# Performance work log

Hardware: AMD Instinct MI355X
Metric: run time of the kernel (lower is better)

## Reference

```python
import jax, jax.numpy as jnp
import numpy as np

NODES = 62        # electrodes per graph (hard-coded in model)
BATCH = 2048      # graphs per batch
N = NODES * BATCH # total nodes
IN = 128          # node feature dim (inchannel)
OUT = 62          # ChebConv out channels (hard-coded)
K = 3             # Chebyshev order (config.K)
LIN = 512         # linearsize
HC = 3            # classes (kwargs['HC'])
EPS = 1e-5        # BatchNorm eps
DEG = 4           # out-neighbors per node before symmetrization


def setup_inputs() -> dict:
    key = jax.random.key(0)
    ks = jax.random.split(key, 24)

    # Block-diagonal batched graph: same random 62-node topology per graph, offset per graph.
    rng = np.random.default_rng(0)
    src = np.repeat(np.arange(NODES), DEG)
    dst = (src + 1 + rng.integers(0, NODES - 1, size=src.shape)) % NODES  # no self-loops
    base = np.stack([np.concatenate([src, dst]), np.concatenate([dst, src])])  # [2, e] symmetric
    offs = (np.arange(BATCH) * NODES)[:, None, None]                            # [B,1,1]
    edge_index = (base[None] + offs).transpose(1, 0, 2).reshape(2, -1)          # [2, E]

    in_dims = [IN, IN + OUT, IN + 2 * OUT, IN + 3 * OUT]
    inp = {
        "x": jax.random.normal(ks[0], (N, IN), dtype=jnp.float32),
        "edge_index": jnp.asarray(edge_index, dtype=jnp.int32),
    }
    for i, d in enumerate(in_dims, start=1):
        inp[f"W{i}"] = jax.random.normal(ks[2 * i], (K, d, OUT), dtype=jnp.float32) * (1.0 / np.sqrt(d))
        inp[f"b{i}"] = jnp.zeros((OUT,), dtype=jnp.float32)
    feat = NODES * 4 * OUT  # 15376
    inp["Wh1"] = jax.random.normal(ks[10], (feat, LIN), dtype=jnp.float32) * (1.0 / np.sqrt(feat))
    inp["bh1"] = jnp.zeros((LIN,), dtype=jnp.float32)
    inp["g1"] = jnp.ones((LIN,), dtype=jnp.float32)
    inp["be1"] = jnp.zeros((LIN,), dtype=jnp.float32)
    inp["Wh2"] = jax.random.normal(ks[11], (LIN, LIN // 2), dtype=jnp.float32) * (1.0 / np.sqrt(LIN))
    inp["bh2"] = jnp.zeros((LIN // 2,), dtype=jnp.float32)
    inp["g2"] = jnp.ones((LIN // 2,), dtype=jnp.float32)
    inp["be2"] = jnp.zeros((LIN // 2,), dtype=jnp.float32)
    inp["Wh3"] = jax.random.normal(ks[12], (LIN // 2, HC), dtype=jnp.float32) * (1.0 / np.sqrt(LIN // 2))
    inp["bh3"] = jnp.zeros((HC,), dtype=jnp.float32)
    return inp


def _batchnorm(h, g, b):
    m = h.mean(axis=0)
    v = h.var(axis=0)  # biased, as torch BN training forward
    return (h - m) * jax.lax.rsqrt(v + EPS) * g + b


def reference(x, edge_index, W1, b1, W2, b2, W3, b3, W4, b4,
              Wh1, bh1, g1, be1, Wh2, bh2, g2, be2, Wh3, bh3):
    n = x.shape[0]
    row, col = edge_index[0], edge_index[1]

    # scaled Laplacian L~ = 2L/lambda_max - I = -D^{-1/2} A D^{-1/2} (sym norm, lambda_max=2)
    deg = jax.ops.segment_sum(jnp.ones(row.shape, x.dtype), row, num_segments=n)
    dinv = jnp.where(deg > 0, jnp.where(deg > 0, deg, 1.0) ** -0.5, 0.0)
    w = -(dinv[row] * dinv[col])  # [E]

    def prop(h):  # L~ @ h via edge scatter/gather
        return jax.ops.segment_sum(w[:, None] * h[col], row, num_segments=n)

    def cheb(h, W, b):  # sum_k T_k(L~) h @ W_k + b
        out = h @ W[0]
        Tx0, Tx1 = h, prop(h)
        out = out + Tx1 @ W[1]
        for k in range(2, W.shape[0]):
            Tx2 = 2.0 * prop(Tx1) - Tx0
            out = out + Tx2 @ W[k]
            Tx0, Tx1 = Tx1, Tx2
        return out + b

    relu = jax.nn.relu
    x1 = relu(cheb(x, W1, b1))
    x2 = relu(cheb(jnp.concatenate([x, x1], axis=1), W2, b2))
    x3 = relu(cheb(jnp.concatenate([x, x1, x2], axis=1), W3, b3))
    x4 = relu(cheb(jnp.concatenate([x, x1, x2, x3], axis=1), W4, b4))

    feats = jnp.concatenate([x1, x2, x3, x4], axis=1)        # [N, 4*OUT]
    feats = feats.reshape(BATCH, -1)                          # [B, 62*4*OUT] (attention==identity)

    h = relu(_batchnorm(feats @ Wh1 + bh1, g1, be1))          # dropout: identity (eval)
    h = relu(_batchnorm(h @ Wh2 + bh2, g2, be2))
    logits = h @ Wh3 + bh3
    return jax.nn.softmax(logits, axis=1)
```

## Files before the change

### kernel.cpp

```cpp
#include <hip/hip_runtime.h>


#define NODES   62
#define BATCH   2048
#define NTOT    (NODES * BATCH)
#define IN_DIM  128
#define OUT_DIM 62
#define ACOLS   248
#define FEAT    15376
#define LIN1    512
#define LIN2    256
#define NCLS    3
#define BN_EPS  1e-5f

typedef __attribute__((ext_vector_type(8)))  short  short8;
typedef __attribute__((ext_vector_type(4)))  float  f32x4;
typedef __attribute__((ext_vector_type(16))) float  f32x16;
typedef __attribute__((ext_vector_type(4)))  unsigned short us4;

__device__ inline unsigned short f2bf(float x) {
    unsigned u = __builtin_bit_cast(unsigned, x);
    return (unsigned short)((u + 0x7fffu + ((u >> 16) & 1u)) >> 16);
}
__device__ inline float bf2f(unsigned short h) {
    return __builtin_bit_cast(float, (unsigned)h << 16);
}
__device__ inline void tsplit(float x, unsigned short& hi, unsigned short& lo) {
    unsigned u = __builtin_bit_cast(unsigned, x);
    hi = (unsigned short)(u >> 16);
    float r = x - __builtin_bit_cast(float, u & 0xffff0000u);
    lo = (unsigned short)(__builtin_bit_cast(unsigned, r) >> 16);
}
__device__ inline int fo(int r, int k) {
    return (((r + 2 * k) & 15) + 16 * k) * 8;
}

#define PREP_GRID 11153
__global__ __launch_bounds__(256) void prep_kernel(
    const int* __restrict__ ei, int E, int epg, unsigned short* __restrict__ Tf,
    const float* __restrict__ W1, const float* __restrict__ W2,
    const float* __restrict__ W3, const float* __restrict__ W4,
    unsigned short* __restrict__ WTall,
    const float* __restrict__ Wh1, unsigned short* __restrict__ Wh1T,
    float* __restrict__ H1, const float* __restrict__ bh1,
    float* __restrict__ H2, const float* __restrict__ bh2)
{
    __shared__ __align__(16) char ps[48640];
    const int bid = blockIdx.x;
    const int t   = threadIdx.x;

    if (bid == 0) {
        float* Ls   = (float*)ps;
        float* Ts   = (float*)(ps + 15376);
        int*   deg  = (int*)(ps + 48144);
        float* dinv = (float*)(ps + 48392);
        for (int i = t; i < NODES * NODES; i += 256) Ls[i] = 0.f;
        if (t < NODES) deg[t] = 0;
        __syncthreads();
        const int* row = ei;
        const int* col = ei + E;
        for (int j = t; j < epg; j += 256) atomicAdd(&deg[row[j]], 1);
        __syncthreads();
        if (t < NODES) dinv[t] = (deg[t] > 0) ? rsqrtf((float)deg[t]) : 0.f;
        __syncthreads();
        for (int j = t; j < epg; j += 256) {
            int r = row[j], c = col[j];
            atomicAdd(&Ls[r * NODES + c], -dinv[r] * dinv[c]);
        }
        __syncthreads();
        for (int idx = t; idx < 4096; idx += 256) {
            int r = idx >> 6, c = idx & 63;
            float t1 = 0.f, t2 = 0.f;
            if (r < NODES && c < NODES) {
                t1 = Ls[r * NODES + c];
                float s = 0.f;
                for (int j = 0; j < NODES; ++j) s += Ls[r * NODES + j] * Ls[j * NODES + c];
                t2 = 2.f * s - (r == c ? 1.f : 0.f);
            }
            Ts[idx]        = t1;
            Ts[4096 + idx] = t2;
        }
        __syncthreads();
        for (int idx = t; idx < 16384; idx += 256) {
            int j    = idx & 7;
            int lane = (idx >> 3) & 63;
            int pl   = (idx >> 9) & 1;
            int ks   = (idx >> 10) & 3;
            int w    = (idx >> 12) & 3;
            int m = (w & 1) * 32 + (lane & 31);
            int k = ks * 16 + (lane >> 5) * 8 + j;
            float v = Ts[(w >> 1) * 4096 + m * 64 + k];
            unsigned short hi, lo;
            tsplit(v, hi, lo);
            Tf[idx] = pl ? lo : hi;
        }
    } else if (bid < 1921) {
        const int li    = bid - 1;
        const int layer = li / 480;
        const int bx    = li - layer * 480;
        const float* W = (layer == 0) ? W1 : (layer == 1) ? W2 : (layer == 2) ? W3 : W4;
        const int d    = (layer == 0) ? 128 : (layer == 1) ? 190 : (layer == 2) ? 252 : 314;
        const int dpad = (layer == 0) ? 128 : (layer == 1) ? 192 : (layer == 2) ? 256 : 320;
        const int cum  = (layer == 0) ? 0 : (layer == 1) ? 4 : (layer == 2) ? 10 : 18;
        unsigned short* WTf = WTall + (size_t)cum * 12288;
        const int total = (dpad >> 5) * 12288;
        int idx = bx * 256 + t;
        if (idx >= total) return;
        int j    = idx & 7;
        int lane = (idx >> 3) & 63;
        int f    = idx >> 9;
        int nt   = f & 1;
        int pl   = (f >> 1) & 1;
        int ks   = (f >> 2) & 1;
        int seg  = (f >> 3) % 3;
        int ch   = (f >> 3) / 3;
        int n  = nt * 32 + (lane & 31);
        int kk = ch * 32 + ks * 16 + (lane >> 5) * 8 + j;
        float v = (n < NODES && kk < d) ? W[((size_t)seg * d + kk) * OUT_DIM + n] : 0.f;
        unsigned short hi, lo;
        tsplit(v, hi, lo);
        WTf[idx] = pl ? lo : hi;
    } else if (bid < 9617) {
        const int ti = bid - 1921;
        const int k0 = (ti % 481) * 32;
        const int n0 = (ti / 481) * 32;
        float (*T)[33] = (float(*)[33])ps;
        {
            int kl = t >> 3, n4 = (t & 7) * 4;
            if (k0 + kl < FEAT) {
                float4 v = *(const float4*)&Wh1[(size_t)(k0 + kl) * LIN1 + n0 + n4];
                T[kl][n4] = v.x; T[kl][n4 + 1] = v.y; T[kl][n4 + 2] = v.z; T[kl][n4 + 3] = v.w;
            }
        }
        __syncthreads();
        {
            int nl = t >> 3, k4 = (t & 7) * 4;
            if (k0 + k4 + 3 < FEAT) {
                ushort4 o;
                o.x = f2bf(T[k4 + 0][nl]);
                o.y = f2bf(T[k4 + 1][nl]);
                o.z = f2bf(T[k4 + 2][nl]);
                o.w = f2bf(T[k4 + 3][nl]);
                *(ushort4*)&Wh1T[(size_t)(n0 + nl) * FEAT + k0 + k4] = o;
            }
        }
    } else {
        const int i = (bid - 9617) * 256 + t;
        const int n1 = BATCH * LIN1 / 4;
        if (i < n1) {
            ((float4*)H1)[i] = ((const float4*)bh1)[i & (LIN1 / 4 - 1)];
        } else {
            int j = i - n1;
            ((float4*)H2)[j] = ((const float4*)bh2)[j & (LIN2 / 4 - 1)];
        }
    }
}

__global__ __launch_bounds__(256, 4) void cheb_mfma(
    const float* __restrict__ x, float* __restrict__ X248,
    const unsigned short* __restrict__ WTf, const unsigned short* __restrict__ Tf,
    const float* __restrict__ bias, int d, int dpad)
{
    __shared__ __align__(16) unsigned short smem[17408];
    __shared__ float bias_s[64];

    unsigned short* hA = smem;
    unsigned short* Bs = smem + 5120;

    const int tid  = threadIdx.x;
    const int g    = blockIdx.x;
    const int lane = tid & 63;
    const int wv   = tid >> 6;
    const int mtw  = wv >> 1, ntw = wv & 1;

    if (tid < 64) bias_s[tid] = (tid < OUT_DIM) ? bias[tid] : 0.f;

    const int srow = tid >> 2;
    const int scg  = (tid & 3) * 8;

    const int nchunk = dpad >> 5;

    f32x16 acc[3];
    #pragma unroll
    for (int s = 0; s < 3; ++s)
        #pragma unroll
        for (int i = 0; i < 16; ++i) acc[s][i] = 0.f;

    float  vh[8];
    short8 breg[6];

#define LOADCH(cn)                                                             \
    do {                                                                       \
        const int gf_ = (cn) * 32 + scg;                                       \
        if (srow < NODES) {                                                    \
            if ((cn) * 32 < IN_DIM) {                                          \
                const float4* p_ = (const float4*)&x[(size_t)(g * NODES + srow) * IN_DIM + gf_]; \
                float4 a_ = p_[0], b_ = p_[1];                                 \
                vh[0] = a_.x; vh[1] = a_.y; vh[2] = a_.z; vh[3] = a_.w;        \
                vh[4] = b_.x; vh[5] = b_.y; vh[6] = b_.z; vh[7] = b_.w;        \
            } else if (gf_ + 8 <= d) {                                         \
                const float4* p_ = (const float4*)&X248[(size_t)(g * NODES + srow) * ACOLS + (gf_ - IN_DIM)]; \
                float4 a_ = p_[0], b_ = p_[1];                                 \
                vh[0] = a_.x; vh[1] = a_.y; vh[2] = a_.z; vh[3] = a_.w;        \
                vh[4] = b_.x; vh[5] = b_.y; vh[6] = b_.z; vh[7] = b_.w;        \
            } else {                                                           \
                _Pragma("unroll")                                              \
                for (int p = 0; p < 8; ++p)                                    \
                    vh[p] = (gf_ + p < d)                                      \
                        ? X248[(size_t)(g * NODES + srow) * ACOLS + (gf_ - IN_DIM) + p] : 0.f; \
            }                                                                  \
        } else {                                                               \
            _Pragma("unroll")                                                  \
            for (int p = 0; p < 8; ++p) vh[p] = 0.f;                           \
        }                                                                      \
        const short8* wsrc_ = (const short8*)(WTf + (size_t)(cn) * 12288);     \
        _Pragma("unroll")                                                      \
        for (int i = 0; i < 6; ++i) breg[i] = wsrc_[i * 256 + tid];            \
    } while (0)

    LOADCH(0);

    for (int ch = 0; ch < nchunk; ++ch) {
        {
            short8 hi8, lo8;
            #pragma unroll
            for (int p = 0; p < 8; ++p) {
                unsigned short h_, l_;
                tsplit(vh[p], h_, l_);
                hi8[p] = (short)h_; lo8[p] = (short)l_;
            }
            *(short8*)&hA[srow * 40 + scg]        = hi8;
            *(short8*)&hA[2560 + srow * 40 + scg] = lo8;
            #pragma unroll
            for (int i = 0; i < 6; ++i) ((short8*)Bs)[i * 256 + tid] = breg[i];
        }
        __syncthreads();
        if (ch + 1 < nchunk) LOADCH(ch + 1);
        {
            const int arow = mtw * 32 + (lane & 31);
            const int akf  = (lane >> 5) * 8;
            #pragma unroll
            for (int ks = 0; ks < 2; ++ks) {
                short8 ahi = *(const short8*)&hA[arow * 40 + ks * 16 + akf];
                short8 alo = *(const short8*)&hA[2560 + arow * 40 + ks * 16 + akf];
                #pragma unroll
                for (int seg = 0; seg < 3; ++seg) {
                    const unsigned short* bp =
                        Bs + ((((seg * 2 + ks) * 2 + 0) * 2 + ntw) << 9) + lane * 8;
                    short8 bhi = *(const short8*)bp;
                    short8 blo = *(const short8*)(bp + 1024);
                    acc[seg] = __builtin_amdgcn_mfma_f32_32x32x16_bf16(ahi, bhi, acc[seg], 0, 0, 0);
                    acc[seg] = __builtin_amdgcn_mfma_f32_32x32x16_bf16(ahi, blo, acc[seg], 0, 0, 0);
                    acc[seg] = __builtin_amdgcn_mfma_f32_32x32x16_bf16(alo, bhi, acc[seg], 0, 0, 0);
                }
            }
        }
        __syncthreads();
    }
#undef LOADCH

    short8 Tr[2][4][2];
    #pragma unroll
    for (int mat = 0; mat < 2; ++mat) {
        const int w = mat * 2 + mtw;
        #pragma unroll
        for (int ks = 0; ks < 4; ++ks)
            #pragma unroll
            for (int pl = 0; pl < 2; ++pl)
                Tr[mat][ks][pl] =
                    *(const short8*)(Tf + (((size_t)(w * 4 + ks) * 2 + pl) << 9) + lane * 8);
    }
    {
        const int jb = (lane >> 5) * 4;
        const int lq = lane & 31;
        #pragma unroll
        for (int q = 0; q < 4; ++q) {
            const int ks2 = mtw * 2 + (q >> 1);
            const int lp  = lq + 32 * (q & 1);
            us4 s1h, s1l, s2h, s2l;
            #pragma unroll
            for (int r = 0; r < 4; ++r) {
                unsigned short hi_, lo_;
                tsplit(acc[1][q * 4 + r], hi_, lo_);
                s1h[r] = hi_; s1l[r] = lo_;
                tsplit(acc[2][q * 4 + r], hi_, lo_);
                s2h[r] = hi_; s2l[r] = lo_;
            }
            const int base = lp * 8 + jb;
            *(us4*)&smem[((((0 + ks2) * 2 + 0) * 2 + ntw) << 9) + base] = s1h;
            *(us4*)&smem[((((0 + ks2) * 2 + 1) * 2 + ntw) << 9) + base] = s1l;
            *(us4*)&smem[((((4 + ks2) * 2 + 0) * 2 + ntw) << 9) + base] = s2h;
            *(us4*)&smem[((((4 + ks2) * 2 + 1) * 2 + ntw) << 9) + base] = s2l;
        }
    }
    __syncthreads();
    f32x16 out = acc[0];
    #pragma unroll
    for (int mat = 0; mat < 2; ++mat)
        #pragma unroll
        for (int ks = 0; ks < 4; ++ks) {
            const unsigned short* sp =
                smem + ((((mat * 4 + ks) * 2 + 0) * 2 + ntw) << 9) + lane * 8;
            short8 shi = *(const short8*)sp;
            short8 slo = *(const short8*)(sp + 1024);
            out = __builtin_amdgcn_mfma_f32_32x32x16_bf16(Tr[mat][ks][0], shi, out, 0, 0, 0);
            out = __builtin_amdgcn_mfma_f32_32x32x16_bf16(Tr[mat][ks][0], slo, out, 0, 0, 0);
            out = __builtin_amdgcn_mfma_f32_32x32x16_bf16(Tr[mat][ks][1], shi, out, 0, 0, 0);
        }
    {
        const int c = ntw * 32 + (lane & 31);
        if (c < OUT_DIM) {
            const int mbase = mtw * 32 + 4 * (lane >> 5);
            #pragma unroll
            for (int reg = 0; reg < 16; ++reg) {
                int m = mbase + (reg & 3) + 8 * (reg >> 2);
                if (m < NODES) {
                    float v = fmaxf(out[reg] + bias_s[c], 0.f);
                    X248[(size_t)(g * NODES + m) * ACOLS + (d - IN_DIM) + c] = v;
                }
            }
        }
    }
}

#define SPLIT1 8
__global__ __launch_bounds__(256) void gemm_head1_mfma(
    const float* __restrict__ F32, const unsigned short* __restrict__ WT1,
    float* __restrict__ H1)
{
    __shared__ __align__(16) unsigned short A16[4 * 512];
    __shared__ __align__(16) unsigned short B16[8 * 512];
    const int tid  = threadIdx.x;
    const int lane = tid & 63;
    const int wv   = tid >> 6;
    const int bm = blockIdx.x, bnb = blockIdx.y, s = blockIdx.z;
    const int c0 = (481 * s) / SPLIT1, c1 = (481 * (s + 1)) / SPLIT1;
    const int mr = tid >> 2, kg = (tid & 3) * 8;
    const int mrB = tid >> 1, kgB = (tid & 1) * 16;
    const int aoff  = (mr >> 4) * 512 + fo(mr & 15, tid & 3);
    const int boff0 = (mrB >> 4) * 512 + fo(mrB & 15, (tid & 1) * 2);
    const int boff1 = (mrB >> 4) * 512 + fo(mrB & 15, (tid & 1) * 2 + 1);
    const int roff  = fo(lane & 15, lane >> 4);

    f32x4 acc[8];
    #pragma unroll
    for (int i = 0; i < 8; ++i) acc[i] = (f32x4){0.f, 0.f, 0.f, 0.f};

    float4 u0, u1;
    short8 bv0, bv1;
#define LOAD1(cn)                                                              \
    do {                                                                       \
        const int k_ = (cn) * 32 + kg;                                         \
        u0 = (float4){0.f, 0.f, 0.f, 0.f};                                     \
        u1 = (float4){0.f, 0.f, 0.f, 0.f};                                     \
        bv0 = (short8){0, 0, 0, 0, 0, 0, 0, 0};                                \
        bv1 = (short8){0, 0, 0, 0, 0, 0, 0, 0};                                \
        if (k_ + 8 <= FEAT) {                                                  \
            const float4* p_ = (const float4*)&F32[(size_t)(bm * 64 + mr) * FEAT + k_]; \
            u0 = p_[0]; u1 = p_[1];                                            \
        }                                                                      \
        const int kB_ = (cn) * 32 + kgB;                                       \
        if (kB_ + 8 <= FEAT)                                                   \
            bv0 = *(const short8*)&WT1[(size_t)(bnb * 128 + mrB) * FEAT + kB_]; \
        if (kB_ + 16 <= FEAT)                                                  \
            bv1 = *(const short8*)&WT1[(size_t)(bnb * 128 + mrB) * FEAT + kB_ + 8]; \
    } while (0)

    LOAD1(c0);
    for (int ch = c0; ch < c1; ++ch) {
        {
            short8 av;
            av[0] = (short)f2bf(u0.x); av[1] = (short)f2bf(u0.y);
            av[2] = (short)f2bf(u0.z); av[3] = (short)f2bf(u0.w);
            av[4] = (short)f2bf(u1.x); av[5] = (short)f2bf(u1.y);
            av[6] = (short)f2bf(u1.z); av[7] = (short)f2bf(u1.w);
            *(short8*)&A16[aoff]  = av;
            *(short8*)&B16[boff0] = bv0;
            *(short8*)&B16[boff1] = bv1;
        }
        __syncthreads();
        if (ch + 1 < c1) LOAD1(ch + 1);
        short8 af = *(short8*)&A16[wv * 512 + roff];
        #pragma unroll
        for (int nt = 0; nt < 8; ++nt) {
            short8 bf = *(short8*)&B16[nt * 512 + roff];
            acc[nt] = __builtin_amdgcn_mfma_f32_16x16x32_bf16(af, bf, acc[nt], 0, 0, 0);
        }
        __syncthreads();
    }
#undef LOAD1
    const int m0 = bm * 64 + wv * 16 + (lane >> 4) * 4;
    #pragma unroll
    for (int nt = 0; nt < 8; ++nt) {
        int c = bnb * 128 + nt * 16 + (lane & 15);
        #pragma unroll
        for (int rg = 0; rg < 4; ++rg)
            atomicAdd(&H1[(size_t)(m0 + rg) * LIN1 + c], acc[nt][rg]);
    }
}

#define ACC16(av, bv) do {                              \
    acc[0][0] = fmaf((av).x, (bv).x, acc[0][0]);        \
    acc[0][1] = fmaf((av).x, (bv).y, acc[0][1]);        \
    acc[0][2] = fmaf((av).x, (bv).z, acc[0][2]);        \
    acc[0][3] = fmaf((av).x, (bv).w, acc[0][3]);        \
    acc[1][0] = fmaf((av).y, (bv).x, acc[1][0]);        \
    acc[1][1] = fmaf((av).y, (bv).y, acc[1][1]);        \
    acc[1][2] = fmaf((av).y, (bv).z, acc[1][2]);        \
    acc[1][3] = fmaf((av).y, (bv).w, acc[1][3]);        \
    acc[2][0] = fmaf((av).z, (bv).x, acc[2][0]);        \
    acc[2][1] = fmaf((av).z, (bv).y, acc[2][1]);        \
    acc[2][2] = fmaf((av).z, (bv).z, acc[2][2]);        \
    acc[2][3] = fmaf((av).z, (bv).w, acc[2][3]);        \
    acc[3][0] = fmaf((av).w, (bv).x, acc[3][0]);        \
    acc[3][1] = fmaf((av).w, (bv).y, acc[3][1]);        \
    acc[3][2] = fmaf((av).w, (bv).z, acc[3][2]);        \
    acc[3][3] = fmaf((av).w, (bv).w, acc[3][3]);        \
} while (0)

#define SPLIT2 4
__global__ __launch_bounds__(256) void gemm2_kernel(
    const float* __restrict__ A, const float* __restrict__ B,
    float* __restrict__ C)
{
    __shared__ __align__(16) float As[16 * 72];
    __shared__ __align__(16) float Bs[16 * 64];
    const int bm = blockIdx.x, bnb = blockIdx.y, s = blockIdx.z;
    const int tid = threadIdx.x;
    const int ty4 = (tid >> 4) * 4;
    const int tx4 = (tid & 15) * 4;
    const int kbeg = s * (LIN1 / SPLIT2);
    const int kend = kbeg + LIN1 / SPLIT2;
    float acc[4][4] = {};
    for (int k0 = kbeg; k0 < kend; k0 += 16) {
        for (int i = tid; i < 1024; i += 256) {
            int m = i >> 4, kt = i & 15;
            As[kt * 72 + m] = A[(size_t)(bm * 64 + m) * LIN1 + k0 + kt];
        }
        for (int i = tid; i < 1024; i += 256) {
            int kt = i >> 6, c = i & 63;
            Bs[kt * 64 + c] = B[(size_t)(k0 + kt) * LIN2 + bnb * 64 + c];
        }
        __syncthreads();
        #pragma unroll
        for (int kt = 0; kt < 16; ++kt) {
            const float4 av = *(const float4*)&As[kt * 72 + ty4];
            const float4 bv = *(const float4*)&Bs[kt * 64 + tx4];
            ACC16(av, bv);
        }
        __syncthreads();
    }
    const int b = bm * 64 + ty4, c = bnb * 64 + tx4;
    #pragma unroll
    for (int i = 0; i < 4; ++i)
        #pragma unroll
        for (int j = 0; j < 4; ++j)
            atomicAdd(&C[(size_t)(b + i) * LIN2 + c + j], acc[i][j]);
}

__global__ __launch_bounds__(256) void bn_relu_kernel(
    float* __restrict__ H, int C,
    const float* __restrict__ gamma, const float* __restrict__ beta)
{
    const int c  = blockIdx.x * 16 + (threadIdx.x & 15);
    const int rt = threadIdx.x >> 4;
    const int ct = threadIdx.x & 15;
    float s = 0.f, s2 = 0.f;
    for (int r = rt; r < BATCH; r += 16) {
        float v = H[(size_t)r * C + c];
        s += v; s2 += v * v;
    }
    __shared__ float Ss[16][16], S2s[16][16], sc_s[16], sh_s[16];
    Ss[rt][ct] = s; S2s[rt][ct] = s2;
    __syncthreads();
    if (rt == 0) {
        float ts = 0.f, ts2 = 0.f;
        #pragma unroll
        for (int i = 0; i < 16; ++i) { ts += Ss[i][ct]; ts2 += S2s[i][ct]; }
        float m   = ts * (1.f / BATCH);
        float var = ts2 * (1.f / BATCH) - m * m;
        float sc  = gamma[c] * rsqrtf(var + BN_EPS);
        sc_s[ct] = sc;
        sh_s[ct] = beta[c] - m * sc;
    }
    __syncthreads();
    const float sc = sc_s[ct], sh = sh_s[ct];
    for (int r = rt; r < BATCH; r += 16) {
        float v = H[(size_t)r * C + c];
        H[(size_t)r * C + c] = fmaxf(fmaf(v, sc, sh), 0.f);
    }
}

__global__ __launch_bounds__(256) void final_kernel(
    const float* __restrict__ H2, const float* __restrict__ Wh3,
    const float* __restrict__ bh3, float* __restrict__ out)
{
    __shared__ float Ws[LIN2 * NCLS];
    __shared__ float bs[NCLS];
    const int tid = threadIdx.x;
    for (int i = tid; i < LIN2 * NCLS; i += 256) Ws[i] = Wh3[i];
    if (tid < NCLS) bs[tid] = bh3[tid];
    __syncthreads();
    const int r = blockIdx.x * 256 + tid;
    float a0 = bs[0], a1 = bs[1], a2 = bs[2];
    const float4* row = (const float4*)&H2[(size_t)r * LIN2];
    for (int k4 = 0; k4 < LIN2 / 4; ++k4) {
        float4 h = row[k4];
        int k = k4 * 4;
        a0 = fmaf(h.x, Ws[(k + 0) * 3 + 0], a0);
        a1 = fmaf(h.x, Ws[(k + 0) * 3 + 1], a1);
        a2 = fmaf(h.x, Ws[(k + 0) * 3 + 2], a2);
        a0 = fmaf(h.y, Ws[(k + 1) * 3 + 0], a0);
        a1 = fmaf(h.y, Ws[(k + 1) * 3 + 1], a1);
        a2 = fmaf(h.y, Ws[(k + 1) * 3 + 2], a2);
        a0 = fmaf(h.z, Ws[(k + 2) * 3 + 0], a0);
        a1 = fmaf(h.z, Ws[(k + 2) * 3 + 1], a1);
        a2 = fmaf(h.z, Ws[(k + 2) * 3 + 2], a2);
        a0 = fmaf(h.w, Ws[(k + 3) * 3 + 0], a0);
        a1 = fmaf(h.w, Ws[(k + 3) * 3 + 1], a1);
        a2 = fmaf(h.w, Ws[(k + 3) * 3 + 2], a2);
    }
    float mx = fmaxf(a0, fmaxf(a1, a2));
    float e0 = expf(a0 - mx), e1 = expf(a1 - mx), e2 = expf(a2 - mx);
    float inv = 1.f / (e0 + e1 + e2);
    out[r * 3 + 0] = e0 * inv;
    out[r * 3 + 1] = e1 * inv;
    out[r * 3 + 2] = e2 * inv;
}

extern "C" void kernel_launch(void* const* d_in, const int* in_sizes, int n_in,
                              void* d_out, int out_size, void* d_ws, size_t ws_size,
                              hipStream_t stream)
{
    const float* x   = (const float*)d_in[0];
    const int*   ei  = (const int*)  d_in[1];
    const float* W1  = (const float*)d_in[2];
    const float* b1  = (const float*)d_in[3];
    const float* W2  = (const float*)d_in[4];
    const float* b2  = (const float*)d_in[5];
    const float* W3  = (const float*)d_in[6];
    const float* b3  = (const float*)d_in[7];
    const float* W4  = (const float*)d_in[8];
    const float* b4  = (const float*)d_in[9];
    const float* Wh1 = (const float*)d_in[10];
    const float* bh1 = (const float*)d_in[11];
    const float* g1  = (const float*)d_in[12];
    const float* be1 = (const float*)d_in[13];
    const float* Wh2 = (const float*)d_in[14];
    const float* bh2 = (const float*)d_in[15];
    const float* g2  = (const float*)d_in[16];
    const float* be2 = (const float*)d_in[17];
    const float* Wh3 = (const float*)d_in[18];
    const float* bh3 = (const float*)d_in[19];
    float* out = (float*)d_out;

    char* ws = (char*)d_ws;
    unsigned short* Tf    = (unsigned short*)(ws + 32768);
    unsigned short* WTall = (unsigned short*)(ws + 65536);
    unsigned short* Wh1T  = (unsigned short*)(ws + 753664);
    float* X248 = (float*)(ws + 16498688);
    float* H1   = (float*)(ws + 142458880);
    float* H2   = (float*)(ws + 146653184);

    const int E   = in_sizes[1] / 2;
    const int epg = E / BATCH;

    prep_kernel<<<PREP_GRID, 256, 0, stream>>>(
        ei, E, epg, Tf, W1, W2, W3, W4, WTall, Wh1, Wh1T, H1, bh1, H2, bh2);

    cheb_mfma<<<BATCH, 256, 0, stream>>>(x, X248, WTall + (size_t)0 * 12288,  Tf, b1, 128, 128);
    cheb_mfma<<<BATCH, 256, 0, stream>>>(x, X248, WTall + (size_t)4 * 12288,  Tf, b2, 190, 192);
    cheb_mfma<<<BATCH, 256, 0, stream>>>(x, X248, WTall + (size_t)10 * 12288, Tf, b3, 252, 256);
    cheb_mfma<<<BATCH, 256, 0, stream>>>(x, X248, WTall + (size_t)18 * 12288, Tf, b4, 314, 320);

    gemm_head1_mfma<<<dim3(32, 4, SPLIT1), 256, 0, stream>>>(X248, Wh1T, H1);
    bn_relu_kernel<<<LIN1 / 16, 256, 0, stream>>>(H1, LIN1, g1, be1);

    gemm2_kernel<<<dim3(32, 4, SPLIT2), 256, 0, stream>>>(H1, Wh2, H2);
    bn_relu_kernel<<<LIN2 / 16, 256, 0, stream>>>(H2, LIN2, g2, be2);

    final_kernel<<<BATCH / 256, 256, 0, stream>>>(H2, Wh3, bh3, out);
}
```

Measured before the change: 639.6 us.

## Fuse four ChebConv layer launches into one per-graph kernel

Replaces the four separate cheb_mfma launches with a single cheb_fused4 kernel that loops over the four layers inside each graph's block, loading all four biases up front. This removes three kernel launches and their inter-kernel drains, and lets each block's earlier-layer outputs in X248 likely still sit in cache when the next layer reads them. The layer loop is unrolled, which may raise code size and register pressure. Correctness relies on each block only reading the X248 rows it wrote itself, with the end-of-layer barrier making them visible.

```diff
diff --git a/kernel.cpp b/kernel.cpp
--- a/kernel.cpp
+++ b/kernel.cpp
@@ -156,13 +156,14 @@
     }
 }
 
-__global__ __launch_bounds__(256, 4) void cheb_mfma(
+__global__ __launch_bounds__(256, 4) void cheb_fused4(
     const float* __restrict__ x, float* __restrict__ X248,
-    const unsigned short* __restrict__ WTf, const unsigned short* __restrict__ Tf,
-    const float* __restrict__ bias, int d, int dpad)
+    const unsigned short* __restrict__ WTall, const unsigned short* __restrict__ Tf,
+    const float* __restrict__ b1, const float* __restrict__ b2,
+    const float* __restrict__ b3, const float* __restrict__ b4)
 {
     __shared__ __align__(16) unsigned short smem[17408];
-    __shared__ float bias_s[64];
+    __shared__ float bias_s[256];
 
     unsigned short* hA = smem;
     unsigned short* Bs = smem + 5120;
@@ -173,21 +174,31 @@
     const int wv   = tid >> 6;
     const int mtw  = wv >> 1, ntw = wv & 1;
 
-    if (tid < 64) bias_s[tid] = (tid < OUT_DIM) ? bias[tid] : 0.f;
+    {
+        const int ll = tid >> 6, c = tid & 63;
+        const float* bp = (ll == 0) ? b1 : (ll == 1) ? b2 : (ll == 2) ? b3 : b4;
+        bias_s[tid] = (c < OUT_DIM) ? bp[c] : 0.f;
+    }
+    __syncthreads();
 
     const int srow = tid >> 2;
     const int scg  = (tid & 3) * 8;
 
-    const int nchunk = dpad >> 5;
-
-    f32x16 acc[3];
     #pragma unroll
-    for (int s = 0; s < 3; ++s)
-        #pragma unroll
-        for (int i = 0; i < 16; ++i) acc[s][i] = 0.f;
-
-    float  vh[8];
-    short8 breg[6];
+    for (int l = 0; l < 4; ++l) {
+        const int d      = (l == 0) ? 128 : (l == 1) ? 190 : (l == 2) ? 252 : 314;
+        const int nchunk = (l == 0) ? 4   : (l == 1) ? 6   : (l == 2) ? 8   : 10;
+        const unsigned short* WTf =
+            WTall + (size_t)((l == 0) ? 0 : (l == 1) ? 4 : (l == 2) ? 10 : 18) * 12288;
+
+        f32x16 acc[3];
+        #pragma unroll
+        for (int s = 0; s < 3; ++s)
+            #pragma unroll
+            for (int i = 0; i < 16; ++i) acc[s][i] = 0.f;
+
+        float  vh[8];
+        short8 breg[6];
 
 #define LOADCH(cn)                                                             \
     do {                                                                       \
@@ -218,108 +229,111 @@
         for (int i = 0; i < 6; ++i) breg[i] = wsrc_[i * 256 + tid];            \
     } while (0)
 
-    LOADCH(0);
-
-    for (int ch = 0; ch < nchunk; ++ch) {
+        LOADCH(0);
+
+        for (int ch = 0; ch < nchunk; ++ch) {
+            {
+                short8 hi8, lo8;
+                #pragma unroll
+                for (int p = 0; p < 8; ++p) {
+                    unsigned short h_, l_;
+                    tsplit(vh[p], h_, l_);
+                    hi8[p] = (short)h_; lo8[p] = (short)l_;
+                }
+                *(short8*)&hA[srow * 40 + scg]        = hi8;
+                *(short8*)&hA[2560 + srow * 40 + scg] = lo8;
+                #pragma unroll
+                for (int i = 0; i < 6; ++i) ((short8*)Bs)[i * 256 + tid] = breg[i];
+            }
+            __syncthreads();
+            if (ch + 1 < nchunk) LOADCH(ch + 1);
+            {
+                const int arow = mtw * 32 + (lane & 31);
+                const int akf  = (lane >> 5) * 8;
+                #pragma unroll
+                for (int ks = 0; ks < 2; ++ks) {
+                    short8 ahi = *(const short8*)&hA[arow * 40 + ks * 16 + akf];
+                    short8 alo = *(const short8*)&hA[2560 + arow * 40 + ks * 16 + akf];
+                    #pragma unroll
+                    for (int seg = 0; seg < 3; ++seg) {
+                        const unsigned short* bp =
+                            Bs + ((((seg * 2 + ks) * 2 + 0) * 2 + ntw) << 9) + lane * 8;
+                        short8 bhi = *(const short8*)bp;
+                        short8 blo = *(const short8*)(bp + 1024);
+                        acc[seg] = __builtin_amdgcn_mfma_f32_32x32x16_bf16(ahi, bhi, acc[seg], 0, 0, 0);
+                        acc[seg] = __builtin_amdgcn_mfma_f32_32x32x16_bf16(ahi, blo, acc[seg], 0, 0, 0);
+                        acc[seg] = __builtin_amdgcn_mfma_f32_32x32x16_bf16(alo, bhi, acc[seg], 0, 0, 0);
+                    }
+                }
+            }
+            __syncthreads();
+        }
+#undef LOADCH
+
+        short8 Tr[2][4][2];
+        #pragma unroll
+        for (int mat = 0; mat < 2; ++mat) {
+            const int w = mat * 2 + mtw;
+            #pragma unroll
+            for (int ks = 0; ks < 4; ++ks)
+                #pragma unroll
+                for (int pl = 0; pl < 2; ++pl)
+                    Tr[mat][ks][pl] =
+                        *(const short8*)(Tf + (((size_t)(w * 4 + ks) * 2 + pl) << 9) + lane * 8);
+        }
         {
-            short8 hi8, lo8;
+            const int jb = (lane >> 5) * 4;
+            const int lq = lane & 31;
             #pragma unroll
-            for (int p = 0; p < 8; ++p) {
-                unsigned short h_, l_;
-                tsplit(vh[p], h_, l_);
-                hi8[p] = (short)h_; lo8[p] = (short)l_;
-            }
-            *(short8*)&hA[srow * 40 + scg]        = hi8;
-            *(short8*)&hA[2560 + srow * 40 + scg] = lo8;
+            for (int q = 0; q < 4; ++q) {
+                const int ks2 = mtw * 2 + (q >> 1);
+                const int lp  = lq + 32 * (q & 1);
+                us4 s1h, s1l, s2h, s2l;
+                #pragma unroll
+                for (int r = 0; r < 4; ++r) {
+                    unsigned short hi_, lo_;
+                    tsplit(acc[1][q * 4 + r], hi_, lo_);
+                    s1h[r] = hi_; s1l[r] = lo_;
+                    tsplit(acc[2][q * 4 + r], hi_, lo_);
+                    s2h[r] = hi_; s2l[r] = lo_;
+                }
+                const int base = lp * 8 + jb;
+                *(us4*)&smem[((((0 + ks2) * 2 + 0) * 2 + ntw) << 9) + base] = s1h;
+                *(us4*)&smem[((((0 + ks2) * 2 + 1) * 2 + ntw) << 9) + base] = s1l;
+                *(us4*)&smem[((((4 + ks2) * 2 + 0) * 2 + ntw) << 9) + base] = s2h;
+                *(us4*)&smem[((((4 + ks2) * 2 + 1) * 2 + ntw) << 9) + base] = s2l;
+            }
+        }
+        __syncthreads();
+        f32x16 outv = acc[0];
+        #pragma unroll
+        for (int mat = 0; mat < 2; ++mat)
             #pragma unroll
-            for (int i = 0; i < 6; ++i) ((short8*)Bs)[i * 256 + tid] = breg[i];
-        }
-        __syncthreads();
-        if (ch + 1 < nchunk) LOADCH(ch + 1);
+            for (int ks = 0; ks < 4; ++ks) {
+                const unsigned short* sp =
+                    smem + ((((mat * 4 + ks) * 2 + 0) * 2 + ntw) << 9) + lane * 8;
+                short8 shi = *(const short8*)sp;
+                short8 slo = *(const short8*)(sp + 1024);
+                outv = __builtin_amdgcn_mfma_f32_32x32x16_bf16(Tr[mat][ks][0], shi, outv, 0, 0, 0);
+                outv = __builtin_amdgcn_mfma_f32_32x32x16_bf16(Tr[mat][ks][0], slo, outv, 0, 0, 0);
+                outv = __builtin_amdgcn_mfma_f32_32x32x16_bf16(Tr[mat][ks][1], shi, outv, 0, 0, 0);
+            }
         {
-            const int arow = mtw * 32 + (lane & 31);
-            const int akf  = (lane >> 5) * 8;
-            #pragma unroll
-            for (int ks = 0; ks < 2; ++ks) {
-                short8 ahi = *(const short8*)&hA[arow * 40 + ks * 16 + akf];
-                short8 alo = *(const short8*)&hA[2560 + arow * 40 + ks * 16 + akf];
+            const int c = ntw * 32 + (lane & 31);
+            if (c < OUT_DIM) {
+                const float bv = bias_s[l * 64 + c];
+                const int mbase = mtw * 32 + 4 * (lane >> 5);
                 #pragma unroll
-                for (int seg = 0; seg < 3; ++seg) {
-                    const unsigned short* bp =
-                        Bs + ((((seg * 2 + ks) * 2 + 0) * 2 + ntw) << 9) + lane * 8;
-                    short8 bhi = *(const short8*)bp;
-                    short8 blo = *(const short8*)(bp + 1024);
-                    acc[seg] = __builtin_amdgcn_mfma_f32_32x32x16_bf16(ahi, bhi, acc[seg], 0, 0, 0);
-                    acc[seg] = __builtin_amdgcn_mfma_f32_32x32x16_bf16(ahi, blo, acc[seg], 0, 0, 0);
-                    acc[seg] = __builtin_amdgcn_mfma_f32_32x32x16_bf16(alo, bhi, acc[seg], 0, 0, 0);
+                for (int reg = 0; reg < 16; ++reg) {
+                    int m = mbase + (reg & 3) + 8 * (reg >> 2);
+                    if (m < NODES) {
+                        float v = fmaxf(outv[reg] + bv, 0.f);
+                        X248[(size_t)(g * NODES + m) * ACOLS + 62 * l + c] = v;
+                    }
                 }
             }
         }
         __syncthreads();
-    }
-#undef LOADCH
-
-    short8 Tr[2][4][2];
-    #pragma unroll
-    for (int mat = 0; mat < 2; ++mat) {
-        const int w = mat * 2 + mtw;
-        #pragma unroll
-        for (int ks = 0; ks < 4; ++ks)
-            #pragma unroll
-            for (int pl = 0; pl < 2; ++pl)
-                Tr[mat][ks][pl] =
-                    *(const short8*)(Tf + (((size_t)(w * 4 + ks) * 2 + pl) << 9) + lane * 8);
-    }
-    {
-        const int jb = (lane >> 5) * 4;
-        const int lq = lane & 31;
-        #pragma unroll
-        for (int q = 0; q < 4; ++q) {
-            const int ks2 = mtw * 2 + (q >> 1);
-            const int lp  = lq + 32 * (q & 1);
-            us4 s1h, s1l, s2h, s2l;
-            #pragma unroll
-            for (int r = 0; r < 4; ++r) {
-                unsigned short hi_, lo_;
-                tsplit(acc[1][q * 4 + r], hi_, lo_);
-                s1h[r] = hi_; s1l[r] = lo_;
-                tsplit(acc[2][q * 4 + r], hi_, lo_);
-                s2h[r] = hi_; s2l[r] = lo_;
-            }
-            const int base = lp * 8 + jb;
-            *(us4*)&smem[((((0 + ks2) * 2 + 0) * 2 + ntw) << 9) + base] = s1h;
-            *(us4*)&smem[((((0 + ks2) * 2 + 1) * 2 + ntw) << 9) + base] = s1l;
-            *(us4*)&smem[((((4 + ks2) * 2 + 0) * 2 + ntw) << 9) + base] = s2h;
-            *(us4*)&smem[((((4 + ks2) * 2 + 1) * 2 + ntw) << 9) + base] = s2l;
-        }
-    }
-    __syncthreads();
-    f32x16 out = acc[0];
-    #pragma unroll
-    for (int mat = 0; mat < 2; ++mat)
-        #pragma unroll
-        for (int ks = 0; ks < 4; ++ks) {
-            const unsigned short* sp =
-                smem + ((((mat * 4 + ks) * 2 + 0) * 2 + ntw) << 9) + lane * 8;
-            short8 shi = *(const short8*)sp;
-            short8 slo = *(const short8*)(sp + 1024);
-            out = __builtin_amdgcn_mfma_f32_32x32x16_bf16(Tr[mat][ks][0], shi, out, 0, 0, 0);
-            out = __builtin_amdgcn_mfma_f32_32x32x16_bf16(Tr[mat][ks][0], slo, out, 0, 0, 0);
-            out = __builtin_amdgcn_mfma_f32_32x32x16_bf16(Tr[mat][ks][1], shi, out, 0, 0, 0);
-        }
-    {
-        const int c = ntw * 32 + (lane & 31);
-        if (c < OUT_DIM) {
-            const int mbase = mtw * 32 + 4 * (lane >> 5);
-            #pragma unroll
-            for (int reg = 0; reg < 16; ++reg) {
-                int m = mbase + (reg & 3) + 8 * (reg >> 2);
-                if (m < NODES) {
-                    float v = fmaxf(out[reg] + bias_s[c], 0.f);
-                    X248[(size_t)(g * NODES + m) * ACOLS + (d - IN_DIM) + c] = v;
-                }
-            }
-        }
     }
 }
 
@@ -568,10 +582,7 @@
     prep_kernel<<<PREP_GRID, 256, 0, stream>>>(
         ei, E, epg, Tf, W1, W2, W3, W4, WTall, Wh1, Wh1T, H1, bh1, H2, bh2);
 
-    cheb_mfma<<<BATCH, 256, 0, stream>>>(x, X248, WTall + (size_t)0 * 12288,  Tf, b1, 128, 128);
-    cheb_mfma<<<BATCH, 256, 0, stream>>>(x, X248, WTall + (size_t)4 * 12288,  Tf, b2, 190, 192);
-    cheb_mfma<<<BATCH, 256, 0, stream>>>(x, X248, WTall + (size_t)10 * 12288, Tf, b3, 252, 256);
-    cheb_mfma<<<BATCH, 256, 0, stream>>>(x, X248, WTall + (size_t)18 * 12288, Tf, b4, 314, 320);
+    cheb_fused4<<<BATCH, 256, 0, stream>>>(x, X248, WTall, Tf, b1, b2, b3, b4);
 
     gemm_head1_mfma<<<dim3(32, 4, SPLIT1), 256, 0, stream>>>(X248, Wh1T, H1);
     bn_relu_kernel<<<LIN1 / 16, 256, 0, stream>>>(H1, LIN1, g1, be1);
```

Result: no change. 647.0 us (+1.2%).

## Split BatchNorm into parallel stats pass and fuse normalize+ReLU into consumers

Applied to the files above, without the earlier changes.

Replaces each bn_relu kernel, which ran few blocks and read and rewrote H in place, with a bn_stats kernel that spreads rows over 16x more blocks and accumulates per-column sums atomically. The normalize+ReLU is applied on the fly when gemm2 loads A and when final_kernel reads H2, so the in-place write pass disappears. final_kernel is also reorganized to use 8 threads per row with shuffle reductions, giving more parallelism. The stats buffers are zeroed by two extra blocks in prep_kernel, which adds atomics and a workspace dependency.

```diff
diff --git a/kernel.cpp b/kernel.cpp
--- a/kernel.cpp
+++ b/kernel.cpp
@@ -35,7 +35,7 @@
     return (((r + 2 * k) & 15) + 16 * k) * 8;
 }
 
-#define PREP_GRID 11153
+#define PREP_GRID 11155
 __global__ __launch_bounds__(256) void prep_kernel(
     const int* __restrict__ ei, int E, int epg, unsigned short* __restrict__ Tf,
     const float* __restrict__ W1, const float* __restrict__ W2,
@@ -43,7 +43,8 @@
     unsigned short* __restrict__ WTall,
     const float* __restrict__ Wh1, unsigned short* __restrict__ Wh1T,
     float* __restrict__ H1, const float* __restrict__ bh1,
-    float* __restrict__ H2, const float* __restrict__ bh2)
+    float* __restrict__ H2, const float* __restrict__ bh2,
+    float* __restrict__ stats)
 {
     __shared__ __align__(16) char ps[48640];
     const int bid = blockIdx.x;
@@ -147,11 +148,16 @@
     } else {
         const int i = (bid - 9617) * 256 + t;
         const int n1 = BATCH * LIN1 / 4;
+        const int n2 = BATCH * LIN2 / 4;
         if (i < n1) {
             ((float4*)H1)[i] = ((const float4*)bh1)[i & (LIN1 / 4 - 1)];
-        } else {
+        } else if (i - n1 < n2) {
             int j = i - n1;
             ((float4*)H2)[j] = ((const float4*)bh2)[j & (LIN2 / 4 - 1)];
+        } else {
+            int j = i - n1 - n2;
+            if (j < 512)
+                ((float4*)stats)[j] = (float4){0.f, 0.f, 0.f, 0.f};
         }
     }
 }
@@ -399,6 +405,31 @@
     }
 }
 
+__global__ __launch_bounds__(256) void bn_stats(
+    const float* __restrict__ H, int C,
+    float* __restrict__ Sg, float* __restrict__ S2g)
+{
+    const int ct = threadIdx.x & 15;
+    const int rt = threadIdx.x >> 4;
+    const int c  = blockIdx.x * 16 + ct;
+    const int r0 = blockIdx.y * 16 + rt;
+    float s = 0.f, s2 = 0.f;
+    for (int r = r0; r < BATCH; r += 256) {
+        float v = H[(size_t)r * C + c];
+        s += v; s2 += v * v;
+    }
+    __shared__ float Ss[16][17], S2s[16][17];
+    Ss[rt][ct] = s; S2s[rt][ct] = s2;
+    __syncthreads();
+    if (rt == 0) {
+        float ts = 0.f, ts2 = 0.f;
+        #pragma unroll
+        for (int i = 0; i < 16; ++i) { ts += Ss[i][ct]; ts2 += S2s[i][ct]; }
+        atomicAdd(&Sg[c], ts);
+        atomicAdd(&S2g[c], ts2);
+    }
+}
+
 #define ACC16(av, bv) do {                              \
     acc[0][0] = fmaf((av).x, (bv).x, acc[0][0]);        \
     acc[0][1] = fmaf((av).x, (bv).y, acc[0][1]);        \
@@ -421,21 +452,35 @@
 #define SPLIT2 4
 __global__ __launch_bounds__(256) void gemm2_kernel(
     const float* __restrict__ A, const float* __restrict__ B,
-    float* __restrict__ C)
+    float* __restrict__ C,
+    const float* __restrict__ Sg1, const float* __restrict__ S2g1,
+    const float* __restrict__ g1, const float* __restrict__ be1)
 {
     __shared__ __align__(16) float As[16 * 72];
     __shared__ __align__(16) float Bs[16 * 64];
+    __shared__ float scs[128], shs[128];
     const int bm = blockIdx.x, bnb = blockIdx.y, s = blockIdx.z;
     const int tid = threadIdx.x;
     const int ty4 = (tid >> 4) * 4;
     const int tx4 = (tid & 15) * 4;
     const int kbeg = s * (LIN1 / SPLIT2);
     const int kend = kbeg + LIN1 / SPLIT2;
+    if (tid < 128) {
+        const int k = kbeg + tid;
+        float mn  = Sg1[k] * (1.f / BATCH);
+        float var = S2g1[k] * (1.f / BATCH) - mn * mn;
+        float sc  = g1[k] * rsqrtf(var + BN_EPS);
+        scs[tid] = sc;
+        shs[tid] = be1[k] - mn * sc;
+    }
+    __syncthreads();
     float acc[4][4] = {};
     for (int k0 = kbeg; k0 < kend; k0 += 16) {
         for (int i = tid; i < 1024; i += 256) {
             int m = i >> 4, kt = i & 15;
-            As[kt * 72 + m] = A[(size_t)(bm * 64 + m) * LIN1 + k0 + kt];
+            float raw = A[(size_t)(bm * 64 + m) * LIN1 + k0 + kt];
+            int kl = k0 + kt - kbeg;
+            As[kt * 72 + m] = fmaxf(fmaf(raw, scs[kl], shs[kl]), 0.f);
         }
         for (int i = tid; i < 1024; i += 256) {
             int kt = i >> 6, c = i & 63;
@@ -458,74 +503,68 @@
             atomicAdd(&C[(size_t)(b + i) * LIN2 + c + j], acc[i][j]);
 }
 
-__global__ __launch_bounds__(256) void bn_relu_kernel(
-    float* __restrict__ H, int C,
-    const float* __restrict__ gamma, const float* __restrict__ beta)
-{
-    const int c  = blockIdx.x * 16 + (threadIdx.x & 15);
-    const int rt = threadIdx.x >> 4;
-    const int ct = threadIdx.x & 15;
-    float s = 0.f, s2 = 0.f;
-    for (int r = rt; r < BATCH; r += 16) {
-        float v = H[(size_t)r * C + c];
-        s += v; s2 += v * v;
-    }
-    __shared__ float Ss[16][16], S2s[16][16], sc_s[16], sh_s[16];
-    Ss[rt][ct] = s; S2s[rt][ct] = s2;
-    __syncthreads();
-    if (rt == 0) {
-        float ts = 0.f, ts2 = 0.f;
-        #pragma unroll
-        for (int i = 0; i < 16; ++i) { ts += Ss[i][ct]; ts2 += S2s[i][ct]; }
-        float m   = ts * (1.f / BATCH);
-        float var = ts2 * (1.f / BATCH) - m * m;
-        float sc  = gamma[c] * rsqrtf(var + BN_EPS);
-        sc_s[ct] = sc;
-        sh_s[ct] = beta[c] - m * sc;
-    }
-    __syncthreads();
-    const float sc = sc_s[ct], sh = sh_s[ct];
-    for (int r = rt; r < BATCH; r += 16) {
-        float v = H[(size_t)r * C + c];
-        H[(size_t)r * C + c] = fmaxf(fmaf(v, sc, sh), 0.f);
-    }
-}
-
 __global__ __launch_bounds__(256) void final_kernel(
     const float* __restrict__ H2, const float* __restrict__ Wh3,
-    const float* __restrict__ bh3, float* __restrict__ out)
+    const float* __restrict__ bh3, float* __restrict__ out,
+    const float* __restrict__ Sg2, const float* __restrict__ S2g2,
+    const float* __restrict__ g2, const float* __restrict__ be2)
 {
     __shared__ float Ws[LIN2 * NCLS];
     __shared__ float bs[NCLS];
+    __shared__ float sc2[LIN2], sh2[LIN2];
     const int tid = threadIdx.x;
     for (int i = tid; i < LIN2 * NCLS; i += 256) Ws[i] = Wh3[i];
     if (tid < NCLS) bs[tid] = bh3[tid];
+    {
+        float mn  = Sg2[tid] * (1.f / BATCH);
+        float var = S2g2[tid] * (1.f / BATCH) - mn * mn;
+        float sc  = g2[tid] * rsqrtf(var + BN_EPS);
+        sc2[tid] = sc;
+        sh2[tid] = be2[tid] - mn * sc;
+    }
     __syncthreads();
-    const int r = blockIdx.x * 256 + tid;
-    float a0 = bs[0], a1 = bs[1], a2 = bs[2];
+    const int r     = blockIdx.x * 32 + (tid >> 3);
+    const int lane8 = tid & 7;
+    float a0 = (lane8 == 0) ? bs[0] : 0.f;
+    float a1 = (lane8 == 0) ? bs[1] : 0.f;
+    float a2 = (lane8 == 0) ? bs[2] : 0.f;
     const float4* row = (const float4*)&H2[(size_t)r * LIN2];
-    for (int k4 = 0; k4 < LIN2 / 4; ++k4) {
+    #pragma unroll
+    for (int i = 0; i < 8; ++i) {
+        const int k4 = lane8 + i * 8;
         float4 h = row[k4];
-        int k = k4 * 4;
-        a0 = fmaf(h.x, Ws[(k + 0) * 3 + 0], a0);
-        a1 = fmaf(h.x, Ws[(k + 0) * 3 + 1], a1);
-        a2 = fmaf(h.x, Ws[(k + 0) * 3 + 2], a2);
-        a0 = fmaf(h.y, Ws[(k + 1) * 3 + 0], a0);
-        a1 = fmaf(h.y, Ws[(k + 1) * 3 + 1], a1);
-        a2 = fmaf(h.y, Ws[(k + 1) * 3 + 2], a2);
-        a0 = fmaf(h.z, Ws[(k + 2) * 3 + 0], a0);
-        a1 = fmaf(h.z, Ws[(k + 2) * 3 + 1], a1);
-        a2 = fmaf(h.z, Ws[(k + 2) * 3 + 2], a2);
-        a0 = fmaf(h.w, Ws[(k + 3) * 3 + 0], a0);
-        a1 = fmaf(h.w, Ws[(k + 3) * 3 + 1], a1);
-        a2 = fmaf(h.w, Ws[(k + 3) * 3 + 2], a2);
-    }
-    float mx = fmaxf(a0, fmaxf(a1, a2));
-    float e0 = expf(a0 - mx), e1 = expf(a1 - mx), e2 = expf(a2 - mx);
-    float inv = 1.f / (e0 + e1 + e2);
-    out[r * 3 + 0] = e0 * inv;
-    out[r * 3 + 1] = e1 * inv;
-    out[r * 3 + 2] = e2 * inv;
+        const int k = k4 * 4;
+        float h0 = fmaxf(fmaf(h.x, sc2[k + 0], sh2[k + 0]), 0.f);
+        float h1 = fmaxf(fmaf(h.y, sc2[k + 1], sh2[k + 1]), 0.f);
+        float h2v = fmaxf(fmaf(h.z, sc2[k + 2], sh2[k + 2]), 0.f);
+        float h3 = fmaxf(fmaf(h.w, sc2[k + 3], sh2[k + 3]), 0.f);
+        a0 = fmaf(h0, Ws[(k + 0) * 3 + 0], a0);
+        a1 = fmaf(h0, Ws[(k + 0) * 3 + 1], a1);
+        a2 = fmaf(h0, Ws[(k + 0) * 3 + 2], a2);
+        a0 = fmaf(h1, Ws[(k + 1) * 3 + 0], a0);
+        a1 = fmaf(h1, Ws[(k + 1) * 3 + 1], a1);
+        a2 = fmaf(h1, Ws[(k + 1) * 3 + 2], a2);
+        a0 = fmaf(h2v, Ws[(k + 2) * 3 + 0], a0);
+        a1 = fmaf(h2v, Ws[(k + 2) * 3 + 1], a1);
+        a2 = fmaf(h2v, Ws[(k + 2) * 3 + 2], a2);
+        a0 = fmaf(h3, Ws[(k + 3) * 3 + 0], a0);
+        a1 = fmaf(h3, Ws[(k + 3) * 3 + 1], a1);
+        a2 = fmaf(h3, Ws[(k + 3) * 3 + 2], a2);
+    }
+    #pragma unroll
+    for (int m = 1; m < 8; m <<= 1) {
+        a0 += __shfl_xor(a0, m);
+        a1 += __shfl_xor(a1, m);
+        a2 += __shfl_xor(a2, m);
+    }
+    if (lane8 == 0) {
+        float mx = fmaxf(a0, fmaxf(a1, a2));
+        float e0 = expf(a0 - mx), e1 = expf(a1 - mx), e2 = expf(a2 - mx);
+        float inv = 1.f / (e0 + e1 + e2);
+        out[r * 3 + 0] = e0 * inv;
+        out[r * 3 + 1] = e1 * inv;
+        out[r * 3 + 2] = e2 * inv;
+    }
 }
 
 extern "C" void kernel_launch(void* const* d_in, const int* in_sizes, int n_in,
@@ -555,6 +594,10 @@
     float* out = (float*)d_out;
 
     char* ws = (char*)d_ws;
+    float* Sg1  = (float*)(ws + 0);
+    float* S2g1 = (float*)(ws + 2048);
+    float* Sg2  = (float*)(ws + 4096);
+    float* S2g2 = (float*)(ws + 5120);
     unsigned short* Tf    = (unsigned short*)(ws + 32768);
     unsigned short* WTall = (unsigned short*)(ws + 65536);
     unsigned short* Wh1T  = (unsigned short*)(ws + 753664);
@@ -566,7 +609,8 @@
     const int epg = E / BATCH;
 
     prep_kernel<<<PREP_GRID, 256, 0, stream>>>(
-        ei, E, epg, Tf, W1, W2, W3, W4, WTall, Wh1, Wh1T, H1, bh1, H2, bh2);
+        ei, E, epg, Tf, W1, W2, W3, W4, WTall, Wh1, Wh1T, H1, bh1, H2, bh2,
+        (float*)ws);
 
     cheb_mfma<<<BATCH, 256, 0, stream>>>(x, X248, WTall + (size_t)0 * 12288,  Tf, b1, 128, 128);
     cheb_mfma<<<BATCH, 256, 0, stream>>>(x, X248, WTall + (size_t)4 * 12288,  Tf, b2, 190, 192);
@@ -574,10 +618,9 @@
     cheb_mfma<<<BATCH, 256, 0, stream>>>(x, X248, WTall + (size_t)18 * 12288, Tf, b4, 314, 320);
 
     gemm_head1_mfma<<<dim3(32, 4, SPLIT1), 256, 0, stream>>>(X248, Wh1T, H1);
-    bn_relu_kernel<<<LIN1 / 16, 256, 0, stream>>>(H1, LIN1, g1, be1);
-
-    gemm2_kernel<<<dim3(32, 4, SPLIT2), 256, 0, stream>>>(H1, Wh2, H2);
-    bn_relu_kernel<<<LIN2 / 16, 256, 0, stream>>>(H2, LIN2, g2, be2);
-
-    final_kernel<<<BATCH / 256, 256, 0, stream>>>(H2, Wh3, bh3, out);
-}
+
+    bn_stats<<<dim3(LIN1 / 16, 16), 256, 0, stream>>>(H1, LIN1, Sg1, S2g1);
+    gemm2_kernel<<<dim3(32, 4, SPLIT2), 256, 0, stream>>>(H1, Wh2, H2, Sg1, S2g1, g1, be1);
+    bn_stats<<<dim3(LIN2 / 16, 16), 256, 0, stream>>>(H2, LIN2, Sg2, S2g2);
+    final_kernel<<<BATCH / 32, 256, 0, stream>>>(H2, Wh3, bh3, out, Sg2, S2g2, g2, be2);
+}
```

After: 518.8 us. -18.9%, faster.
